# Kernel tuning notes

Hardware: AMD Instinct MI355X
Metric: run time of the kernel (lower is better)

The kernel has to match this reference:

```python
import jax, jax.numpy as jnp
import numpy as np

B, S, D = 2, 4096, 512
H, DK, DV = 8, 64, 64
LN_EPS = 1e-5
ATTN_EPS = 1e-6


def layer_norm(x, g, b):
    mu = jnp.mean(x, axis=-1, keepdims=True)
    var = jnp.var(x, axis=-1, keepdims=True)
    return (x - mu) * jax.lax.rsqrt(var + LN_EPS) * g + b


def setup_inputs() -> dict:
    key = jax.random.key(0)
    ks = jax.random.split(key, 12)
    s = 1.0 / np.sqrt(D)
    inp = {
        "Q": jax.random.normal(ks[0], (B, S, D), jnp.float32),
        "K": jax.random.normal(ks[1], (B, S, D), jnp.float32),
        "V": jax.random.normal(ks[2], (B, S, D), jnp.float32),
        "W_q": jax.random.normal(ks[3], (D, H * DK), jnp.float32) * s,
        "W_k": jax.random.normal(ks[4], (D, H * DK), jnp.float32) * s,
        "W_v": jax.random.normal(ks[5], (D, H * DV), jnp.float32) * s,
        "W_o": jax.random.normal(ks[6], (H * DV, D), jnp.float32) * s,
        "ln1_g": jnp.ones((D,), jnp.float32),
        "ln1_b": jnp.zeros((D,), jnp.float32),
        "ln2_g": jnp.ones((D,), jnp.float32),
        "ln2_b": jnp.zeros((D,), jnp.float32),
        "w1": jax.random.normal(ks[7], (4 * D, D), jnp.float32) * s,  # torch Linear: (out, in)
        "b1": jnp.zeros((4 * D,), jnp.float32),
        "w2": jax.random.normal(ks[8], (D, 4 * D), jnp.float32) * (1.0 / np.sqrt(4 * D)),
        "b2": jnp.zeros((D,), jnp.float32),
    }
    return inp


def reference(Q, K, V, W_q, W_k, W_v, W_o, ln1_g, ln1_b, ln2_g, ln2_b, w1, b1, w2, b2):
    Qn = layer_norm(Q, ln1_g, ln1_b)
    # project and split heads: [B,S,H,dk] -> [B,H,S,dk]
    q = (Qn @ W_q).reshape(B, S, H, DK).transpose(0, 2, 1, 3)
    k = (K @ W_k).reshape(B, S, H, DK).transpose(0, 2, 1, 3)
    v = (V @ W_v).reshape(B, S, H, DV).transpose(0, 2, 1, 3)
    scores = jnp.einsum("bhqd,bhkd->bhqk", q, k) / (np.sqrt(DK) + ATTN_EPS)
    attn = jax.nn.softmax(scores, axis=-1)  # same as max-subtract softmax
    ctx = jnp.einsum("bhqk,bhkd->bhqd", attn, v)
    ctx = ctx.transpose(0, 2, 1, 3).reshape(B, S, H * DV)
    att_out = ctx @ W_o  # dropout = identity (eval)
    X = Q + att_out
    Xn = layer_norm(X, ln2_g, ln2_b)
    h = jax.nn.gelu(Xn @ w1.T + b1, approximate=False)
    ffn = h @ w2.T + b2
    return X + ffn
```

## Files before the change

kernel.cpp:

```cpp
#include <hip/hip_runtime.h>

typedef unsigned short u16;
typedef __attribute__((ext_vector_type(8))) short short8;
typedef __attribute__((ext_vector_type(4))) float f32x4;
typedef __attribute__((ext_vector_type(16))) float f32x16;
typedef __attribute__((ext_vector_type(4))) unsigned u32x4;

struct __align__(8) us4 { u16 x, y, z, w; };
struct __align__(8) ui2 { unsigned x, y; };

#define CEXP (1.44269504089f / (8.0f + 1e-6f))

__device__ __forceinline__ u16 f2bf(float f) {
  unsigned u = __builtin_bit_cast(unsigned, f);
  unsigned r = (u + 0x7FFFu + ((u >> 16) & 1u)) >> 16;
  return (u16)r;
}

__device__ __forceinline__ unsigned pack_bf2_trunc(float a, float b) {
  return __builtin_amdgcn_perm(__builtin_bit_cast(unsigned, b),
                               __builtin_bit_cast(unsigned, a), 0x07060302u);
}

__device__ __forceinline__ void async_load16(const void* g, void* l) {
  __builtin_amdgcn_global_load_lds((const __attribute__((address_space(1))) void*)g,
                                   (__attribute__((address_space(3))) void*)l, 16, 0, 0);
}

__global__ void prep_weights(const float* __restrict__ Wq, const float* __restrict__ Wk,
                             const float* __restrict__ Wv, const float* __restrict__ Wo,
                             const float* __restrict__ w1, const float* __restrict__ w2,
                             u16* __restrict__ wqkvT, u16* __restrict__ woT,
                             u16* __restrict__ w1b, u16* __restrict__ w2b) {
  const int z = blockIdx.y;
  const int stride = gridDim.x * blockDim.x;
  const int i0 = blockIdx.x * blockDim.x + threadIdx.x;
  if (z < 4) {
    const float* src = z == 0 ? Wq : z == 1 ? Wk : z == 2 ? Wv : Wo;
    u16* dst = z < 3 ? wqkvT + z * 512 * 512 : woT;
    const float scale = (z == 0) ? CEXP : 1.0f;
    for (int i = i0; i < 512 * 512; i += stride) {
      int n = i >> 9, k = i & 511;
      dst[i] = f2bf(src[k * 512 + n] * scale);
    }
  } else {
    const float* src = z == 4 ? w1 : w2;
    u16* dst = z == 4 ? w1b : w2b;
    for (int i = i0; i < 2048 * 512; i += stride) dst[i] = f2bf(src[i]);
  }
}

template <bool KV>
__launch_bounds__(128)
__global__ void ln_cast(const float* __restrict__ X, const float* __restrict__ gw,
                        const float* __restrict__ bw, u16* __restrict__ Y,
                        const float* __restrict__ Kin, const float* __restrict__ Vin,
                        u16* __restrict__ Kb, u16* __restrict__ Vb) {
  const int row = blockIdx.x, t = threadIdx.x;
  const size_t base = (size_t)row * 512;
  float4 x = ((const float4*)(X + base))[t];
  float s = x.x + x.y + x.z + x.w;
  float ss = x.x * x.x + x.y * x.y + x.z * x.z + x.w * x.w;
#pragma unroll
  for (int off = 32; off > 0; off >>= 1) {
    s += __shfl_xor(s, off);
    ss += __shfl_xor(ss, off);
  }
  __shared__ float red[4];
  if ((t & 63) == 0) { red[(t >> 6) * 2] = s; red[(t >> 6) * 2 + 1] = ss; }
  __syncthreads();
  const float tot = red[0] + red[2], tss = red[1] + red[3];
  const float mu = tot * (1.0f / 512.0f);
  const float var = tss * (1.0f / 512.0f) - mu * mu;
  const float rs = rsqrtf(var + 1e-5f);
  float4 g4 = ((const float4*)gw)[t];
  float4 b4 = ((const float4*)bw)[t];
  us4 o;
  o.x = f2bf((x.x - mu) * rs * g4.x + b4.x);
  o.y = f2bf((x.y - mu) * rs * g4.y + b4.y);
  o.z = f2bf((x.z - mu) * rs * g4.z + b4.z);
  o.w = f2bf((x.w - mu) * rs * g4.w + b4.w);
  ((us4*)(Y + base))[t] = o;
  if constexpr (KV) {
    float4 k4 = ((const float4*)(Kin + base))[t];
    float4 v4 = ((const float4*)(Vin + base))[t];
    us4 ko, vo;
    ko.x = f2bf(k4.x); ko.y = f2bf(k4.y); ko.z = f2bf(k4.z); ko.w = f2bf(k4.w);
    vo.x = f2bf(v4.x); vo.y = f2bf(v4.y); vo.z = f2bf(v4.z); vo.w = f2bf(v4.w);
    ((us4*)(Kb + base))[t] = ko;
    ((us4*)(Vb + base))[t] = vo;
  }
}

__launch_bounds__(256, 3)
__global__ void gemm_qkv(const u16* __restrict__ Aq, const u16* __restrict__ Ak,
                         const u16* __restrict__ Av, const u16* __restrict__ Bt,
                         u16* __restrict__ qb, u16* __restrict__ kb, u16* __restrict__ vtb) {
  __shared__ __align__(16) u16 sA[128 * 32];
  __shared__ __align__(16) u16 sB[128 * 32];
  const int tid = threadIdx.x;
  const int wave = tid >> 6, lane = tid & 63;
  const int l15 = lane & 15, quad = lane >> 4;
  const int qsw = (quad ^ ((l15 >> 1) & 3)) * 8;
  const int m0 = blockIdx.x * 128, n0 = blockIdx.y * 128;
  const int sel = n0 >> 9;
  const u16* A = sel == 0 ? Aq : sel == 1 ? Ak : Av;
  const int wm = (wave >> 1) * 64, wn = (wave & 1) * 64;
  const int u0 = wave * 64 + lane, u1 = u0 + 256;
  const int sw0 = ((u0 & 3) ^ ((u0 >> 3) & 3)) * 8;
  const int K = 512;

  const u16* a0 = A + (size_t)(m0 + (u0 >> 2)) * K + sw0;
  const u16* a1 = A + (size_t)(m0 + (u1 >> 2)) * K + sw0;
  const u16* b0 = Bt + (size_t)(n0 + (u0 >> 2)) * K + sw0;
  const u16* b1p = Bt + (size_t)(n0 + (u1 >> 2)) * K + sw0;

  f32x4 acc[4][4] = {};
  for (int k0 = 0; k0 < K; k0 += 32) {
    async_load16(a0 + k0, &sA[wave * 512]);
    async_load16(a1 + k0, &sA[2048 + wave * 512]);
    async_load16(b0 + k0, &sB[wave * 512]);
    async_load16(b1p + k0, &sB[2048 + wave * 512]);
    __syncthreads();
    short8 af[4], bfr[4];
#pragma unroll
    for (int i = 0; i < 4; i++)
      af[i] = *(const short8*)&sA[(wm + i * 16 + l15) * 32 + qsw];
#pragma unroll
    for (int j = 0; j < 4; j++)
      bfr[j] = *(const short8*)&sB[(wn + j * 16 + l15) * 32 + qsw];
#pragma unroll
    for (int i = 0; i < 4; i++)
#pragma unroll
      for (int j = 0; j < 4; j++)
        acc[i][j] = __builtin_amdgcn_mfma_f32_16x16x32_bf16(af[i], bfr[j], acc[i][j], 0, 0, 0);
    __syncthreads();
  }

#pragma unroll
  for (int i = 0; i < 4; i++) {
#pragma unroll
    for (int j = 0; j < 4; j++) {
      const int ocol = ((n0 + wn) & 511) + j * 16 + l15;
      const int row0 = m0 + wm + i * 16 + quad * 4;
      if (sel < 2) {
        u16* C = sel == 0 ? qb : kb;
#pragma unroll
        for (int r = 0; r < 4; r++) C[(size_t)(row0 + r) * 512 + ocol] = f2bf(acc[i][j][r]);
      } else {
        const int b = row0 >> 12, s0 = row0 & 4095;
        const int hh = ocol >> 6, cc = ocol & 63;
        us4 pk;
        pk.x = f2bf(acc[i][j][0]); pk.y = f2bf(acc[i][j][1]);
        pk.z = f2bf(acc[i][j][2]); pk.w = f2bf(acc[i][j][3]);
        *(us4*)&vtb[((size_t)((b * 8 + hh) * 64 + cc) << 12) + s0] = pk;
      }
    }
  }
}

template <int EP, int TN, int LB>
__launch_bounds__(256, LB)
__global__ void gemm_bt(const u16* __restrict__ A, const u16* __restrict__ Bt,
                        int M, int N, int K, void* __restrict__ Cp,
                        const float* __restrict__ bias, const float* __restrict__ res) {
  constexpr int MI = (TN == 128) ? 4 : 2;
  __shared__ __align__(16) u16 sA[128 * 32];
  __shared__ __align__(16) u16 sB[TN * 32];
  const int tid = threadIdx.x;
  const int wave = tid >> 6, lane = tid & 63;
  const int l15 = lane & 15, quad = lane >> 4;
  const int qsw = (quad ^ ((l15 >> 1) & 3)) * 8;
  const int m0 = blockIdx.x * 128, n0 = blockIdx.y * TN;
  const int wm = (TN == 128) ? (wave >> 1) * 64 : wave * 32;
  const int wn = (TN == 128) ? (wave & 1) * 64 : 0;
  const int u0 = wave * 64 + lane, u1 = u0 + 256;
  const int sw0 = ((u0 & 3) ^ ((u0 >> 3) & 3)) * 8;

  const u16* a0 = A + (size_t)(m0 + (u0 >> 2)) * K + sw0;
  const u16* a1 = A + (size_t)(m0 + (u1 >> 2)) * K + sw0;
  const u16* b0 = Bt + (size_t)(n0 + (u0 >> 2)) * K + sw0;

  f32x4 acc[MI][4] = {};
  for (int k0 = 0; k0 < K; k0 += 32) {
    async_load16(a0 + k0, &sA[wave * 512]);
    async_load16(a1 + k0, &sA[2048 + wave * 512]);
    async_load16(b0 + k0, &sB[wave * 512]);
    if constexpr (TN == 128) {
      const u16* b1p = Bt + (size_t)(n0 + (u1 >> 2)) * K + sw0;
      async_load16(b1p + k0, &sB[2048 + wave * 512]);
    }
    __syncthreads();
    short8 af[MI], bfr[4];
#pragma unroll
    for (int i = 0; i < MI; i++)
      af[i] = *(const short8*)&sA[(wm + i * 16 + l15) * 32 + qsw];
#pragma unroll
    for (int j = 0; j < 4; j++)
      bfr[j] = *(const short8*)&sB[(wn + j * 16 + l15) * 32 + qsw];
#pragma unroll
    for (int i = 0; i < MI; i++)
#pragma unroll
      for (int j = 0; j < 4; j++)
        acc[i][j] = __builtin_amdgcn_mfma_f32_16x16x32_bf16(af[i], bfr[j], acc[i][j], 0, 0, 0);
    __syncthreads();
  }

#pragma unroll
  for (int i = 0; i < MI; i++) {
#pragma unroll
    for (int j = 0; j < 4; j++) {
      const int col = n0 + wn + j * 16 + l15;
      const int row0 = m0 + wm + i * 16 + quad * 4;
      if (EP == 2) {
        float* C = (float*)Cp;
#pragma unroll
        for (int r = 0; r < 4; r++) {
          size_t idx = (size_t)(row0 + r) * N + col;
          C[idx] = acc[i][j][r] + res[idx];
        }
      } else if (EP == 3) {
        u16* C = (u16*)Cp;
        const float bv = bias[col];
#pragma unroll
        for (int r = 0; r < 4; r++) {
          float xx = acc[i][j][r] + bv;
          float gl = 0.5f * xx * (1.0f + erff(xx * 0.70710678118f));
          C[(size_t)(row0 + r) * N + col] = f2bf(gl);
        }
      } else {
        float* C = (float*)Cp;
        const float bv = bias[col];
#pragma unroll
        for (int r = 0; r < 4; r++) {
          size_t idx = (size_t)(row0 + r) * N + col;
          C[idx] = acc[i][j][r] + bv + res[idx];
        }
      }
    }
  }
}

__launch_bounds__(512, 4)
__global__ void attn_kernel(const u16* __restrict__ qb, const u16* __restrict__ kb,
                            const u16* __restrict__ vtb, u16* __restrict__ ctx) {
  __shared__ __align__(16) u16 sK[2][128 * 64];
  __shared__ __align__(16) u16 sV[2][64 * 128];
  const int tid = threadIdx.x;
  const int wave = tid >> 6, lane = tid & 63;
  const int l31 = lane & 31, hi = lane >> 5;
  const int qg = wave & 3, kh = wave >> 2;
  const int bh = blockIdx.y, b = bh >> 3, h = bh & 7;
  const int q0 = blockIdx.x * 128;
  const size_t rb = (size_t)b * 4096;
  const int qrow = q0 + qg * 32 + l31;

  short8 qf[4];
#pragma unroll
  for (int ks = 0; ks < 4; ks++)
    qf[ks] = *(const short8*)&qb[(rb + qrow) * 512 + h * 64 + ks * 16 + hi * 8];

#define STAGE(bufidx, jj)                                                            \
  {                                                                                  \
    _Pragma("unroll") for (int r = 0; r < 2; r++) {                                  \
      int u = r * 512 + wave * 64 + lane;                                            \
      int row = u >> 3, sl = (u & 7) ^ (row & 7);                                    \
      async_load16(&kb[(rb + (jj) + row) * 512 + h * 64 + sl * 8],                   \
                   &sK[bufidx][(r * 512 + wave * 64) * 8]);                          \
    }                                                                                \
    _Pragma("unroll") for (int r = 0; r < 2; r++) {                                  \
      int u = r * 512 + wave * 64 + lane;                                            \
      int row = u >> 4, sl = (u & 15) ^ (row & 7);                                   \
      async_load16(&vtb[((size_t)(bh * 64 + row)) * 4096 + (jj) + sl * 8],           \
                   &sV[bufidx][(r * 512 + wave * 64) * 8]);                          \
    }                                                                                \
  }

  f32x16 ov[2] = {};
  float l_part = 0.f;

  STAGE(0, 0);
  asm volatile("s_waitcnt vmcnt(0)" ::: "memory");
  __syncthreads();

  for (int t = 0; t < 32; t++) {
    const int cur = t & 1;
    if (t < 31) STAGE(cur ^ 1, (t + 1) * 128);
    const u16* K_ = sK[cur];
    const u16* V_ = sV[cur];
#pragma unroll
    for (int kk2 = 0; kk2 < 2; kk2++) {
      const int kb32 = kh * 2 + kk2;
      f32x16 st = {};
      __builtin_amdgcn_s_setprio(1);
#pragma unroll
      for (int ks = 0; ks < 4; ks++) {
        const int row = kb32 * 32 + l31;
        const int sl = (ks * 2 + hi) ^ (row & 7);
        short8 kf = *(const short8*)&K_[row * 64 + sl * 8];
        st = __builtin_amdgcn_mfma_f32_32x32x16_bf16(kf, qf[ks], st, 0, 0, 0);
      }
      __builtin_amdgcn_s_setprio(0);
      float p[16];
#pragma unroll
      for (int i = 0; i < 16; i++) p[i] = __builtin_amdgcn_exp2f(st[i]);
#pragma unroll
      for (int i = 0; i < 16; i += 4)
        l_part += (p[i] + p[i + 1]) + (p[i + 2] + p[i + 3]);
      unsigned x0 = pack_bf2_trunc(p[0], p[1]), x1 = pack_bf2_trunc(p[2], p[3]);
      unsigned x2 = pack_bf2_trunc(p[4], p[5]), x3 = pack_bf2_trunc(p[6], p[7]);
      unsigned x4 = pack_bf2_trunc(p[8], p[9]), x5 = pack_bf2_trunc(p[10], p[11]);
      unsigned x6 = pack_bf2_trunc(p[12], p[13]), x7 = pack_bf2_trunc(p[14], p[15]);
      auto r0 = __builtin_amdgcn_permlane32_swap(x0, x2, false, false);
      auto r1 = __builtin_amdgcn_permlane32_swap(x1, x3, false, false);
      auto r2 = __builtin_amdgcn_permlane32_swap(x4, x6, false, false);
      auto r3 = __builtin_amdgcn_permlane32_swap(x5, x7, false, false);
      u32x4 w0 = {r0[0], r1[0], r0[1], r1[1]};
      u32x4 w1 = {r2[0], r3[0], r2[1], r3[1]};
      short8 pf0 = __builtin_bit_cast(short8, w0);
      short8 pf1 = __builtin_bit_cast(short8, w1);
      __builtin_amdgcn_s_setprio(1);
#pragma unroll
      for (int vb = 0; vb < 2; vb++) {
        const int row = vb * 32 + l31;
        const int sl0 = (kb32 * 4 + hi) ^ (row & 7);
        const int sl1 = (kb32 * 4 + 2 + hi) ^ (row & 7);
        short8 vf0 = *(const short8*)&V_[row * 128 + sl0 * 8];
        short8 vf1 = *(const short8*)&V_[row * 128 + sl1 * 8];
        ov[vb] = __builtin_amdgcn_mfma_f32_32x32x16_bf16(vf0, pf0, ov[vb], 0, 0, 0);
        ov[vb] = __builtin_amdgcn_mfma_f32_32x32x16_bf16(vf1, pf1, ov[vb], 0, 0, 0);
      }
      __builtin_amdgcn_s_setprio(0);
    }
    asm volatile("s_waitcnt vmcnt(0)" ::: "memory");
    __syncthreads();
  }
#undef STAGE

  float l2 = l_part + __shfl_xor(l_part, 32);
  float* mrg = (float*)&sK[0][0];
  float* mrgl = (float*)&sV[0][0];
  if (kh == 1) {
#pragma unroll
    for (int vb = 0; vb < 2; vb++)
#pragma unroll
      for (int e = 0; e < 16; e++)
        mrg[(qg * 32 + vb * 16 + e) * 64 + lane] = ov[vb][e];
    mrgl[qg * 64 + lane] = l2;
  }
  __syncthreads();
  if (kh == 0) {
    const float inv = 1.0f / (l2 + mrgl[qg * 64 + lane]);
#pragma unroll
    for (int vb = 0; vb < 2; vb++) {
#pragma unroll
      for (int rg = 0; rg < 4; rg++) {
        us4 o;
        o.x = f2bf((ov[vb][rg * 4 + 0] + mrg[(qg * 32 + vb * 16 + rg * 4 + 0) * 64 + lane]) * inv);
        o.y = f2bf((ov[vb][rg * 4 + 1] + mrg[(qg * 32 + vb * 16 + rg * 4 + 1) * 64 + lane]) * inv);
        o.z = f2bf((ov[vb][rg * 4 + 2] + mrg[(qg * 32 + vb * 16 + rg * 4 + 2) * 64 + lane]) * inv);
        o.w = f2bf((ov[vb][rg * 4 + 3] + mrg[(qg * 32 + vb * 16 + rg * 4 + 3) * 64 + lane]) * inv);
        *(us4*)&ctx[(rb + qrow) * 512 + h * 64 + vb * 32 + rg * 8 + hi * 4] = o;
      }
    }
  }
}

extern "C" void kernel_launch(void* const* d_in, const int* in_sizes, int n_in,
                              void* d_out, int out_size, void* d_ws, size_t ws_size,
                              hipStream_t stream) {
  (void)in_sizes; (void)n_in; (void)out_size; (void)ws_size;
  const float* Q = (const float*)d_in[0];
  const float* K = (const float*)d_in[1];
  const float* V = (const float*)d_in[2];
  const float* W_q = (const float*)d_in[3];
  const float* W_k = (const float*)d_in[4];
  const float* W_v = (const float*)d_in[5];
  const float* W_o = (const float*)d_in[6];
  const float* ln1_g = (const float*)d_in[7];
  const float* ln1_b = (const float*)d_in[8];
  const float* ln2_g = (const float*)d_in[9];
  const float* ln2_b = (const float*)d_in[10];
  const float* w1 = (const float*)d_in[11];
  const float* b1 = (const float*)d_in[12];
  const float* w2 = (const float*)d_in[13];
  const float* b2 = (const float*)d_in[14];

  char* w = (char*)d_ws;
  const size_t MB = 1u << 20;
  u16* wqkvT = (u16*)(w);
  u16* woT = (u16*)(w + 3 * MB / 2);
  u16* w1b = (u16*)(w + 2 * MB);
  u16* w2b = (u16*)(w + 4 * MB);
  u16* Qn  = (u16*)(w + 6 * MB);
  u16* Kb  = (u16*)(w + 14 * MB);
  u16* Vb  = (u16*)(w + 22 * MB);
  u16* qb  = (u16*)(w + 30 * MB);
  u16* kb  = (u16*)(w + 38 * MB);
  u16* vtb = (u16*)(w + 46 * MB);
  u16* ctx = (u16*)(w + 54 * MB);
  float* X = (float*)(w + 62 * MB);
  u16* Xn  = (u16*)(w + 6 * MB);
  u16* hb  = (u16*)(w + 14 * MB);

  prep_weights<<<dim3(128, 6), 256, 0, stream>>>(W_q, W_k, W_v, W_o, w1, w2,
                                                 wqkvT, woT, w1b, w2b);
  ln_cast<true><<<8192, 128, 0, stream>>>(Q, ln1_g, ln1_b, Qn, K, V, Kb, Vb);
  gemm_qkv<<<dim3(64, 12), 256, 0, stream>>>(Qn, Kb, Vb, wqkvT, qb, kb, vtb);
  attn_kernel<<<dim3(32, 16), 512, 0, stream>>>(qb, kb, vtb, ctx);
  gemm_bt<2, 64, 3><<<dim3(64, 8), 256, 0, stream>>>(ctx, woT, 8192, 512, 512, X, nullptr, Q);
  ln_cast<false><<<8192, 128, 0, stream>>>(X, ln2_g, ln2_b, Xn, nullptr, nullptr, nullptr, nullptr);
  gemm_bt<3, 128, 3><<<dim3(64, 16), 256, 0, stream>>>(Xn, w1b, 8192, 2048, 512, hb, b1, nullptr);
  gemm_bt<4, 64, 3><<<dim3(64, 8), 256, 0, stream>>>(hb, w2b, 8192, 512, 2048, (float*)d_out, b2, X);
}
```

Baseline: 335.1 us.

## Double query rows per attention block and triple-buffer K/V staging

Each wave in the attention kernel now processes two 32-row query tiles (256 queries per block), so every K/V fragment read from shared memory feeds twice as many MFMAs. The grid is halved and launch bounds are relaxed to allow more registers. K/V staging moves to a three-deep ring with precomputed pointers and partial vmcnt waits, giving loads an extra iteration of lead time. The cost is higher register and LDS use and fewer blocks, which lowers occupancy and may leave CUs idle with only 256 blocks.

```diff
diff --git a/kernel.cpp b/kernel.cpp
--- a/kernel.cpp
+++ b/kernel.cpp
@@ -241,126 +241,169 @@
   }
 }
 
-__launch_bounds__(512, 4)
+__launch_bounds__(512, 2)
 __global__ void attn_kernel(const u16* __restrict__ qb, const u16* __restrict__ kb,
                             const u16* __restrict__ vtb, u16* __restrict__ ctx) {
-  __shared__ __align__(16) u16 sK[2][128 * 64];
-  __shared__ __align__(16) u16 sV[2][64 * 128];
+  __shared__ __align__(16) u16 smem[49152];
   const int tid = threadIdx.x;
   const int wave = tid >> 6, lane = tid & 63;
   const int l31 = lane & 31, hi = lane >> 5;
   const int qg = wave & 3, kh = wave >> 2;
   const int bh = blockIdx.y, b = bh >> 3, h = bh & 7;
-  const int q0 = blockIdx.x * 128;
+  const int q0 = blockIdx.x * 256;
   const size_t rb = (size_t)b * 4096;
-  const int qrow = q0 + qg * 32 + l31;
-
-  short8 qf[4];
-#pragma unroll
-  for (int ks = 0; ks < 4; ks++)
-    qf[ks] = *(const short8*)&qb[(rb + qrow) * 512 + h * 64 + ks * 16 + hi * 8];
-
-#define STAGE(bufidx, jj)                                                            \
-  {                                                                                  \
-    _Pragma("unroll") for (int r = 0; r < 2; r++) {                                  \
-      int u = r * 512 + wave * 64 + lane;                                            \
-      int row = u >> 3, sl = (u & 7) ^ (row & 7);                                    \
-      async_load16(&kb[(rb + (jj) + row) * 512 + h * 64 + sl * 8],                   \
-                   &sK[bufidx][(r * 512 + wave * 64) * 8]);                          \
-    }                                                                                \
-    _Pragma("unroll") for (int r = 0; r < 2; r++) {                                  \
-      int u = r * 512 + wave * 64 + lane;                                            \
-      int row = u >> 4, sl = (u & 15) ^ (row & 7);                                   \
-      async_load16(&vtb[((size_t)(bh * 64 + row)) * 4096 + (jj) + sl * 8],           \
-                   &sV[bufidx][(r * 512 + wave * 64) * 8]);                          \
-    }                                                                                \
-  }
-
-  f32x16 ov[2] = {};
-  float l_part = 0.f;
-
-  STAGE(0, 0);
-  asm volatile("s_waitcnt vmcnt(0)" ::: "memory");
+  const int qrowA = q0 + qg * 64 + l31;
+  const int qrowB = qrowA + 32;
+
+  short8 qfA[4], qfB[4];
+#pragma unroll
+  for (int ks = 0; ks < 4; ks++) {
+    qfA[ks] = *(const short8*)&qb[(rb + qrowA) * 512 + h * 64 + ks * 16 + hi * 8];
+    qfB[ks] = *(const short8*)&qb[(rb + qrowB) * 512 + h * 64 + ks * 16 + hi * 8];
+  }
+
+  const int uk0 = wave * 64 + lane, uk1 = uk0 + 512;
+  const int krow0 = uk0 >> 3, ksl0 = (uk0 & 7) ^ (krow0 & 7);
+  const int krow1 = uk1 >> 3, ksl1 = (uk1 & 7) ^ (krow1 & 7);
+  const u16* kp0 = kb + (rb + krow0) * 512 + h * 64 + ksl0 * 8;
+  const u16* kp1 = kb + (rb + krow1) * 512 + h * 64 + ksl1 * 8;
+  const int vrow0 = uk0 >> 4, vsl0 = (uk0 & 15) ^ (vrow0 & 7);
+  const int vrow1 = uk1 >> 4, vsl1 = (uk1 & 15) ^ (vrow1 & 7);
+  const u16* vp0 = vtb + (size_t)(bh * 64 + vrow0) * 4096 + vsl0 * 8;
+  const u16* vp1 = vtb + (size_t)(bh * 64 + vrow1) * 4096 + vsl1 * 8;
+
+#define STAGE(bi)                                                   \
+  {                                                                 \
+    u16* dK = smem + (bi) * 8192;                                   \
+    u16* dV = smem + 24576 + (bi) * 8192;                           \
+    async_load16(kp0, &dK[(wave * 64) * 8]);                        \
+    async_load16(kp1, &dK[(512 + wave * 64) * 8]);                  \
+    async_load16(vp0, &dV[(wave * 64) * 8]);                        \
+    async_load16(vp1, &dV[(512 + wave * 64) * 8]);                  \
+    kp0 += 128 * 512; kp1 += 128 * 512; vp0 += 128; vp1 += 128;     \
+  }
+
+  f32x16 ovA[2] = {}, ovB[2] = {};
+  float lA = 0.f, lB = 0.f;
+
+  STAGE(0);
+  STAGE(1);
+  asm volatile("s_waitcnt vmcnt(4)" ::: "memory");
   __syncthreads();
 
   for (int t = 0; t < 32; t++) {
-    const int cur = t & 1;
-    if (t < 31) STAGE(cur ^ 1, (t + 1) * 128);
-    const u16* K_ = sK[cur];
-    const u16* V_ = sV[cur];
+    const int cur = t % 3;
+    if (t < 30) STAGE((t + 2) % 3);
+    const u16* K_ = smem + cur * 8192;
+    const u16* V_ = smem + 24576 + cur * 8192;
 #pragma unroll
     for (int kk2 = 0; kk2 < 2; kk2++) {
       const int kb32 = kh * 2 + kk2;
-      f32x16 st = {};
+      f32x16 stA = {}, stB = {};
       __builtin_amdgcn_s_setprio(1);
 #pragma unroll
       for (int ks = 0; ks < 4; ks++) {
         const int row = kb32 * 32 + l31;
-        const int sl = (ks * 2 + hi) ^ (row & 7);
+        const int sl = (ks * 2 + hi) ^ (l31 & 7);
         short8 kf = *(const short8*)&K_[row * 64 + sl * 8];
-        st = __builtin_amdgcn_mfma_f32_32x32x16_bf16(kf, qf[ks], st, 0, 0, 0);
+        stA = __builtin_amdgcn_mfma_f32_32x32x16_bf16(kf, qfA[ks], stA, 0, 0, 0);
+        stB = __builtin_amdgcn_mfma_f32_32x32x16_bf16(kf, qfB[ks], stB, 0, 0, 0);
       }
       __builtin_amdgcn_s_setprio(0);
-      float p[16];
-#pragma unroll
-      for (int i = 0; i < 16; i++) p[i] = __builtin_amdgcn_exp2f(st[i]);
-#pragma unroll
-      for (int i = 0; i < 16; i += 4)
-        l_part += (p[i] + p[i + 1]) + (p[i + 2] + p[i + 3]);
-      unsigned x0 = pack_bf2_trunc(p[0], p[1]), x1 = pack_bf2_trunc(p[2], p[3]);
-      unsigned x2 = pack_bf2_trunc(p[4], p[5]), x3 = pack_bf2_trunc(p[6], p[7]);
-      unsigned x4 = pack_bf2_trunc(p[8], p[9]), x5 = pack_bf2_trunc(p[10], p[11]);
-      unsigned x6 = pack_bf2_trunc(p[12], p[13]), x7 = pack_bf2_trunc(p[14], p[15]);
-      auto r0 = __builtin_amdgcn_permlane32_swap(x0, x2, false, false);
-      auto r1 = __builtin_amdgcn_permlane32_swap(x1, x3, false, false);
-      auto r2 = __builtin_amdgcn_permlane32_swap(x4, x6, false, false);
-      auto r3 = __builtin_amdgcn_permlane32_swap(x5, x7, false, false);
-      u32x4 w0 = {r0[0], r1[0], r0[1], r1[1]};
-      u32x4 w1 = {r2[0], r3[0], r2[1], r3[1]};
-      short8 pf0 = __builtin_bit_cast(short8, w0);
-      short8 pf1 = __builtin_bit_cast(short8, w1);
+      float pA[16], pB[16];
+#pragma unroll
+      for (int i = 0; i < 16; i++) pA[i] = __builtin_amdgcn_exp2f(stA[i]);
+#pragma unroll
+      for (int i = 0; i < 16; i++) pB[i] = __builtin_amdgcn_exp2f(stB[i]);
+#pragma unroll
+      for (int i = 0; i < 16; i += 4) {
+        lA += (pA[i] + pA[i + 1]) + (pA[i + 2] + pA[i + 3]);
+        lB += (pB[i] + pB[i + 1]) + (pB[i + 2] + pB[i + 3]);
+      }
+      unsigned a0 = pack_bf2_trunc(pA[0], pA[1]), a1 = pack_bf2_trunc(pA[2], pA[3]);
+      unsigned a2 = pack_bf2_trunc(pA[4], pA[5]), a3 = pack_bf2_trunc(pA[6], pA[7]);
+      unsigned a4 = pack_bf2_trunc(pA[8], pA[9]), a5 = pack_bf2_trunc(pA[10], pA[11]);
+      unsigned a6 = pack_bf2_trunc(pA[12], pA[13]), a7 = pack_bf2_trunc(pA[14], pA[15]);
+      auto ra0 = __builtin_amdgcn_permlane32_swap(a0, a2, false, false);
+      auto ra1 = __builtin_amdgcn_permlane32_swap(a1, a3, false, false);
+      auto ra2 = __builtin_amdgcn_permlane32_swap(a4, a6, false, false);
+      auto ra3 = __builtin_amdgcn_permlane32_swap(a5, a7, false, false);
+      u32x4 wa0 = {ra0[0], ra1[0], ra0[1], ra1[1]};
+      u32x4 wa1 = {ra2[0], ra3[0], ra2[1], ra3[1]};
+      short8 pfA0 = __builtin_bit_cast(short8, wa0);
+      short8 pfA1 = __builtin_bit_cast(short8, wa1);
+      unsigned b0 = pack_bf2_trunc(pB[0], pB[1]), b1 = pack_bf2_trunc(pB[2], pB[3]);
+      unsigned b2 = pack_bf2_trunc(pB[4], pB[5]), b3 = pack_bf2_trunc(pB[6], pB[7]);
+      unsigned b4 = pack_bf2_trunc(pB[8], pB[9]), b5 = pack_bf2_trunc(pB[10], pB[11]);
+      unsigned b6 = pack_bf2_trunc(pB[12], pB[13]), b7 = pack_bf2_trunc(pB[14], pB[15]);
+      auto rb0 = __builtin_amdgcn_permlane32_swap(b0, b2, false, false);
+      auto rb1 = __builtin_amdgcn_permlane32_swap(b1, b3, false, false);
+      auto rb2 = __builtin_amdgcn_permlane32_swap(b4, b6, false, false);
+      auto rb3 = __builtin_amdgcn_permlane32_swap(b5, b7, false, false);
+      u32x4 wb0 = {rb0[0], rb1[0], rb0[1], rb1[1]};
+      u32x4 wb1 = {rb2[0], rb3[0], rb2[1], rb3[1]};
+      short8 pfB0 = __builtin_bit_cast(short8, wb0);
+      short8 pfB1 = __builtin_bit_cast(short8, wb1);
       __builtin_amdgcn_s_setprio(1);
 #pragma unroll
       for (int vb = 0; vb < 2; vb++) {
         const int row = vb * 32 + l31;
-        const int sl0 = (kb32 * 4 + hi) ^ (row & 7);
-        const int sl1 = (kb32 * 4 + 2 + hi) ^ (row & 7);
+        const int sl0 = (kb32 * 4 + hi) ^ (l31 & 7);
+        const int sl1 = (kb32 * 4 + 2 + hi) ^ (l31 & 7);
         short8 vf0 = *(const short8*)&V_[row * 128 + sl0 * 8];
         short8 vf1 = *(const short8*)&V_[row * 128 + sl1 * 8];
-        ov[vb] = __builtin_amdgcn_mfma_f32_32x32x16_bf16(vf0, pf0, ov[vb], 0, 0, 0);
-        ov[vb] = __builtin_amdgcn_mfma_f32_32x32x16_bf16(vf1, pf1, ov[vb], 0, 0, 0);
+        ovA[vb] = __builtin_amdgcn_mfma_f32_32x32x16_bf16(vf0, pfA0, ovA[vb], 0, 0, 0);
+        ovA[vb] = __builtin_amdgcn_mfma_f32_32x32x16_bf16(vf1, pfA1, ovA[vb], 0, 0, 0);
+        ovB[vb] = __builtin_amdgcn_mfma_f32_32x32x16_bf16(vf0, pfB0, ovB[vb], 0, 0, 0);
+        ovB[vb] = __builtin_amdgcn_mfma_f32_32x32x16_bf16(vf1, pfB1, ovB[vb], 0, 0, 0);
       }
       __builtin_amdgcn_s_setprio(0);
     }
-    asm volatile("s_waitcnt vmcnt(0)" ::: "memory");
-    __syncthreads();
+    if (t < 31) {
+      if (t < 30)
+        asm volatile("s_waitcnt vmcnt(4)" ::: "memory");
+      else
+        asm volatile("s_waitcnt vmcnt(0)" ::: "memory");
+      __syncthreads();
+    }
   }
 #undef STAGE
 
-  float l2 = l_part + __shfl_xor(l_part, 32);
-  float* mrg = (float*)&sK[0][0];
-  float* mrgl = (float*)&sV[0][0];
+  float l2A = lA + __shfl_xor(lA, 32);
+  float l2B = lB + __shfl_xor(lB, 32);
+  __syncthreads();
+  float* mrg = (float*)&smem[0];
+  float* mrgl = (float*)&smem[32768];
   if (kh == 1) {
 #pragma unroll
     for (int vb = 0; vb < 2; vb++)
 #pragma unroll
-      for (int e = 0; e < 16; e++)
-        mrg[(qg * 32 + vb * 16 + e) * 64 + lane] = ov[vb][e];
-    mrgl[qg * 64 + lane] = l2;
+      for (int e = 0; e < 16; e++) {
+        mrg[((qg * 2 + 0) * 32 + vb * 16 + e) * 64 + lane] = ovA[vb][e];
+        mrg[((qg * 2 + 1) * 32 + vb * 16 + e) * 64 + lane] = ovB[vb][e];
+      }
+    mrgl[(qg * 2 + 0) * 64 + lane] = l2A;
+    mrgl[(qg * 2 + 1) * 64 + lane] = l2B;
   }
   __syncthreads();
   if (kh == 0) {
-    const float inv = 1.0f / (l2 + mrgl[qg * 64 + lane]);
+    const float invA = 1.0f / (l2A + mrgl[(qg * 2 + 0) * 64 + lane]);
+    const float invB = 1.0f / (l2B + mrgl[(qg * 2 + 1) * 64 + lane]);
 #pragma unroll
     for (int vb = 0; vb < 2; vb++) {
 #pragma unroll
       for (int rg = 0; rg < 4; rg++) {
-        us4 o;
-        o.x = f2bf((ov[vb][rg * 4 + 0] + mrg[(qg * 32 + vb * 16 + rg * 4 + 0) * 64 + lane]) * inv);
-        o.y = f2bf((ov[vb][rg * 4 + 1] + mrg[(qg * 32 + vb * 16 + rg * 4 + 1) * 64 + lane]) * inv);
-        o.z = f2bf((ov[vb][rg * 4 + 2] + mrg[(qg * 32 + vb * 16 + rg * 4 + 2) * 64 + lane]) * inv);
-        o.w = f2bf((ov[vb][rg * 4 + 3] + mrg[(qg * 32 + vb * 16 + rg * 4 + 3) * 64 + lane]) * inv);
-        *(us4*)&ctx[(rb + qrow) * 512 + h * 64 + vb * 32 + rg * 8 + hi * 4] = o;
+        us4 oA, oB;
+        oA.x = f2bf((ovA[vb][rg * 4 + 0] + mrg[((qg * 2 + 0) * 32 + vb * 16 + rg * 4 + 0) * 64 + lane]) * invA);
+        oA.y = f2bf((ovA[vb][rg * 4 + 1] + mrg[((qg * 2 + 0) * 32 + vb * 16 + rg * 4 + 1) * 64 + lane]) * invA);
+        oA.z = f2bf((ovA[vb][rg * 4 + 2] + mrg[((qg * 2 + 0) * 32 + vb * 16 + rg * 4 + 2) * 64 + lane]) * invA);
+        oA.w = f2bf((ovA[vb][rg * 4 + 3] + mrg[((qg * 2 + 0) * 32 + vb * 16 + rg * 4 + 3) * 64 + lane]) * invA);
+        *(us4*)&ctx[(rb + qrowA) * 512 + h * 64 + vb * 32 + rg * 8 + hi * 4] = oA;
+        oB.x = f2bf((ovB[vb][rg * 4 + 0] + mrg[((qg * 2 + 1) * 32 + vb * 16 + rg * 4 + 0) * 64 + lane]) * invB);
+        oB.y = f2bf((ovB[vb][rg * 4 + 1] + mrg[((qg * 2 + 1) * 32 + vb * 16 + rg * 4 + 1) * 64 + lane]) * invB);
+        oB.z = f2bf((ovB[vb][rg * 4 + 2] + mrg[((qg * 2 + 1) * 32 + vb * 16 + rg * 4 + 2) * 64 + lane]) * invB);
+        oB.w = f2bf((ovB[vb][rg * 4 + 3] + mrg[((qg * 2 + 1) * 32 + vb * 16 + rg * 4 + 3) * 64 + lane]) * invB);
+        *(us4*)&ctx[(rb + qrowB) * 512 + h * 64 + vb * 32 + rg * 8 + hi * 4] = oB;
       }
     }
   }
@@ -407,7 +450,7 @@
                                                  wqkvT, woT, w1b, w2b);
   ln_cast<true><<<8192, 128, 0, stream>>>(Q, ln1_g, ln1_b, Qn, K, V, Kb, Vb);
   gemm_qkv<<<dim3(64, 12), 256, 0, stream>>>(Qn, Kb, Vb, wqkvT, qb, kb, vtb);
-  attn_kernel<<<dim3(32, 16), 512, 0, stream>>>(qb, kb, vtb, ctx);
+  attn_kernel<<<dim3(16, 16), 512, 0, stream>>>(qb, kb, vtb, ctx);
   gemm_bt<2, 64, 3><<<dim3(64, 8), 256, 0, stream>>>(ctx, woT, 8192, 512, 512, X, nullptr, Q);
   ln_cast<false><<<8192, 128, 0, stream>>>(X, ln2_g, ln2_b, Xn, nullptr, nullptr, nullptr, nullptr);
   gemm_bt<3, 128, 3><<<dim3(64, 16), 256, 0, stream>>>(Xn, w1b, 8192, 2048, 512, hb, b1, nullptr);
```

Result: faster. 322.8 us (-3.7%).

## Triple-buffer attention K/V tiles in 64-key chunks with wait-one prefetch

Applied to the files above, without the earlier changes.

Restructures the attention kernel's K/V staging from double-buffered 128-key tiles to triple-buffered 64-key tiles. The loop now waits only on the oldest outstanding load (vmcnt(2)) so two prefetches stay in flight. The wave mapping changes so each wave handles 32 keys per tile, and the grid axes are swapped so consecutive blocks share a head. It also lowers the launch-bounds occupancy hint from 4 to 2, which relaxes the register limit but adds one barrier per 64 keys, twice as many as before.

```diff
diff --git a/kernel.cpp b/kernel.cpp
--- a/kernel.cpp
+++ b/kernel.cpp
@@ -241,17 +241,16 @@
   }
 }
 
-__launch_bounds__(512, 4)
+__launch_bounds__(512, 2)
 __global__ void attn_kernel(const u16* __restrict__ qb, const u16* __restrict__ kb,
                             const u16* __restrict__ vtb, u16* __restrict__ ctx) {
-  __shared__ __align__(16) u16 sK[2][128 * 64];
-  __shared__ __align__(16) u16 sV[2][64 * 128];
+  __shared__ __align__(16) u16 smem[24576];
   const int tid = threadIdx.x;
   const int wave = tid >> 6, lane = tid & 63;
   const int l31 = lane & 31, hi = lane >> 5;
-  const int qg = wave & 3, kh = wave >> 2;
-  const int bh = blockIdx.y, b = bh >> 3, h = bh & 7;
-  const int q0 = blockIdx.x * 128;
+  const int qg = wave >> 1, kh = wave & 1;
+  const int bh = blockIdx.x, b = bh >> 3, h = bh & 7;
+  const int q0 = blockIdx.y * 128;
   const size_t rb = (size_t)b * 4096;
   const int qrow = q0 + qg * 32 + l31;
 
@@ -260,86 +259,88 @@
   for (int ks = 0; ks < 4; ks++)
     qf[ks] = *(const short8*)&qb[(rb + qrow) * 512 + h * 64 + ks * 16 + hi * 8];
 
-#define STAGE(bufidx, jj)                                                            \
-  {                                                                                  \
-    _Pragma("unroll") for (int r = 0; r < 2; r++) {                                  \
-      int u = r * 512 + wave * 64 + lane;                                            \
-      int row = u >> 3, sl = (u & 7) ^ (row & 7);                                    \
-      async_load16(&kb[(rb + (jj) + row) * 512 + h * 64 + sl * 8],                   \
-                   &sK[bufidx][(r * 512 + wave * 64) * 8]);                          \
-    }                                                                                \
-    _Pragma("unroll") for (int r = 0; r < 2; r++) {                                  \
-      int u = r * 512 + wave * 64 + lane;                                            \
-      int row = u >> 4, sl = (u & 15) ^ (row & 7);                                   \
-      async_load16(&vtb[((size_t)(bh * 64 + row)) * 4096 + (jj) + sl * 8],           \
-                   &sV[bufidx][(r * 512 + wave * 64) * 8]);                          \
-    }                                                                                \
+  const int srow = tid >> 3, ssl = (tid & 7) ^ (srow & 7);
+  const u16* kp = kb + (rb + srow) * 512 + h * 64 + ssl * 8;
+  const u16* vp = vtb + (size_t)(bh * 64 + srow) * 4096 + ssl * 8;
+
+#define STAGE(bi)                                  \
+  {                                                \
+    async_load16(kp, &smem[(bi) * 4096 + tid * 8]);\
+    async_load16(vp, &smem[12288 + (bi) * 4096 + tid * 8]); \
+    kp += 64 * 512; vp += 64;                      \
   }
 
   f32x16 ov[2] = {};
   float l_part = 0.f;
 
-  STAGE(0, 0);
-  asm volatile("s_waitcnt vmcnt(0)" ::: "memory");
+  STAGE(0);
+  STAGE(1);
+  asm volatile("s_waitcnt vmcnt(2)" ::: "memory");
   __syncthreads();
 
-  for (int t = 0; t < 32; t++) {
-    const int cur = t & 1;
-    if (t < 31) STAGE(cur ^ 1, (t + 1) * 128);
-    const u16* K_ = sK[cur];
-    const u16* V_ = sV[cur];
-#pragma unroll
-    for (int kk2 = 0; kk2 < 2; kk2++) {
-      const int kb32 = kh * 2 + kk2;
-      f32x16 st = {};
-      __builtin_amdgcn_s_setprio(1);
-#pragma unroll
-      for (int ks = 0; ks < 4; ks++) {
-        const int row = kb32 * 32 + l31;
-        const int sl = (ks * 2 + hi) ^ (row & 7);
-        short8 kf = *(const short8*)&K_[row * 64 + sl * 8];
-        st = __builtin_amdgcn_mfma_f32_32x32x16_bf16(kf, qf[ks], st, 0, 0, 0);
-      }
-      __builtin_amdgcn_s_setprio(0);
-      float p[16];
-#pragma unroll
-      for (int i = 0; i < 16; i++) p[i] = __builtin_amdgcn_exp2f(st[i]);
-#pragma unroll
-      for (int i = 0; i < 16; i += 4)
-        l_part += (p[i] + p[i + 1]) + (p[i + 2] + p[i + 3]);
-      unsigned x0 = pack_bf2_trunc(p[0], p[1]), x1 = pack_bf2_trunc(p[2], p[3]);
-      unsigned x2 = pack_bf2_trunc(p[4], p[5]), x3 = pack_bf2_trunc(p[6], p[7]);
-      unsigned x4 = pack_bf2_trunc(p[8], p[9]), x5 = pack_bf2_trunc(p[10], p[11]);
-      unsigned x6 = pack_bf2_trunc(p[12], p[13]), x7 = pack_bf2_trunc(p[14], p[15]);
-      auto r0 = __builtin_amdgcn_permlane32_swap(x0, x2, false, false);
-      auto r1 = __builtin_amdgcn_permlane32_swap(x1, x3, false, false);
-      auto r2 = __builtin_amdgcn_permlane32_swap(x4, x6, false, false);
-      auto r3 = __builtin_amdgcn_permlane32_swap(x5, x7, false, false);
-      u32x4 w0 = {r0[0], r1[0], r0[1], r1[1]};
-      u32x4 w1 = {r2[0], r3[0], r2[1], r3[1]};
-      short8 pf0 = __builtin_bit_cast(short8, w0);
-      short8 pf1 = __builtin_bit_cast(short8, w1);
-      __builtin_amdgcn_s_setprio(1);
-#pragma unroll
-      for (int vb = 0; vb < 2; vb++) {
-        const int row = vb * 32 + l31;
-        const int sl0 = (kb32 * 4 + hi) ^ (row & 7);
-        const int sl1 = (kb32 * 4 + 2 + hi) ^ (row & 7);
-        short8 vf0 = *(const short8*)&V_[row * 128 + sl0 * 8];
-        short8 vf1 = *(const short8*)&V_[row * 128 + sl1 * 8];
-        ov[vb] = __builtin_amdgcn_mfma_f32_32x32x16_bf16(vf0, pf0, ov[vb], 0, 0, 0);
-        ov[vb] = __builtin_amdgcn_mfma_f32_32x32x16_bf16(vf1, pf1, ov[vb], 0, 0, 0);
-      }
-      __builtin_amdgcn_s_setprio(0);
-    }
-    asm volatile("s_waitcnt vmcnt(0)" ::: "memory");
-    __syncthreads();
+  int cur = 0, nxt = 2;
+  for (int t = 0; t < 64; t++) {
+    if (t < 62) {
+      STAGE(nxt);
+      nxt = nxt == 2 ? 0 : nxt + 1;
+    }
+    const u16* K_ = smem + cur * 4096;
+    const u16* V_ = smem + 12288 + cur * 4096;
+    cur = cur == 2 ? 0 : cur + 1;
+    f32x16 st = {};
+    __builtin_amdgcn_s_setprio(1);
+#pragma unroll
+    for (int ks = 0; ks < 4; ks++) {
+      const int row = kh * 32 + l31;
+      const int sl = (ks * 2 + hi) ^ (row & 7);
+      short8 kf = *(const short8*)&K_[row * 64 + sl * 8];
+      st = __builtin_amdgcn_mfma_f32_32x32x16_bf16(kf, qf[ks], st, 0, 0, 0);
+    }
+    __builtin_amdgcn_s_setprio(0);
+    float p[16];
+#pragma unroll
+    for (int i = 0; i < 16; i++) p[i] = __builtin_amdgcn_exp2f(st[i]);
+#pragma unroll
+    for (int i = 0; i < 16; i += 4)
+      l_part += (p[i] + p[i + 1]) + (p[i + 2] + p[i + 3]);
+    unsigned x0 = pack_bf2_trunc(p[0], p[1]), x1 = pack_bf2_trunc(p[2], p[3]);
+    unsigned x2 = pack_bf2_trunc(p[4], p[5]), x3 = pack_bf2_trunc(p[6], p[7]);
+    unsigned x4 = pack_bf2_trunc(p[8], p[9]), x5 = pack_bf2_trunc(p[10], p[11]);
+    unsigned x6 = pack_bf2_trunc(p[12], p[13]), x7 = pack_bf2_trunc(p[14], p[15]);
+    auto r0 = __builtin_amdgcn_permlane32_swap(x0, x2, false, false);
+    auto r1 = __builtin_amdgcn_permlane32_swap(x1, x3, false, false);
+    auto r2 = __builtin_amdgcn_permlane32_swap(x4, x6, false, false);
+    auto r3 = __builtin_amdgcn_permlane32_swap(x5, x7, false, false);
+    u32x4 w0 = {r0[0], r1[0], r0[1], r1[1]};
+    u32x4 w1 = {r2[0], r3[0], r2[1], r3[1]};
+    short8 pf0 = __builtin_bit_cast(short8, w0);
+    short8 pf1 = __builtin_bit_cast(short8, w1);
+    __builtin_amdgcn_s_setprio(1);
+#pragma unroll
+    for (int vb = 0; vb < 2; vb++) {
+      const int row = vb * 32 + l31;
+      const int sl0 = (kh * 4 + hi) ^ (row & 7);
+      const int sl1 = (kh * 4 + 2 + hi) ^ (row & 7);
+      short8 vf0 = *(const short8*)&V_[row * 64 + sl0 * 8];
+      short8 vf1 = *(const short8*)&V_[row * 64 + sl1 * 8];
+      ov[vb] = __builtin_amdgcn_mfma_f32_32x32x16_bf16(vf0, pf0, ov[vb], 0, 0, 0);
+      ov[vb] = __builtin_amdgcn_mfma_f32_32x32x16_bf16(vf1, pf1, ov[vb], 0, 0, 0);
+    }
+    __builtin_amdgcn_s_setprio(0);
+    if (t < 63) {
+      if (t < 62)
+        asm volatile("s_waitcnt vmcnt(2)" ::: "memory");
+      else
+        asm volatile("s_waitcnt vmcnt(0)" ::: "memory");
+      __syncthreads();
+    }
   }
 #undef STAGE
 
   float l2 = l_part + __shfl_xor(l_part, 32);
-  float* mrg = (float*)&sK[0][0];
-  float* mrgl = (float*)&sV[0][0];
+  __syncthreads();
+  float* mrg = (float*)smem;
+  float* mrgl = (float*)smem + 8192;
   if (kh == 1) {
 #pragma unroll
     for (int vb = 0; vb < 2; vb++)
@@ -407,7 +408,7 @@
                                                  wqkvT, woT, w1b, w2b);
   ln_cast<true><<<8192, 128, 0, stream>>>(Q, ln1_g, ln1_b, Qn, K, V, Kb, Vb);
   gemm_qkv<<<dim3(64, 12), 256, 0, stream>>>(Qn, Kb, Vb, wqkvT, qb, kb, vtb);
-  attn_kernel<<<dim3(32, 16), 512, 0, stream>>>(qb, kb, vtb, ctx);
+  attn_kernel<<<dim3(16, 32), 512, 0, stream>>>(qb, kb, vtb, ctx);
   gemm_bt<2, 64, 3><<<dim3(64, 8), 256, 0, stream>>>(ctx, woT, 8192, 512, 512, X, nullptr, Q);
   ln_cast<false><<<8192, 128, 0, stream>>>(X, ln2_g, ln2_b, Xn, nullptr, nullptr, nullptr, nullptr);
   gemm_bt<3, 128, 3><<<dim3(64, 16), 256, 0, stream>>>(Xn, w1b, 8192, 2048, 512, hb, b1, nullptr);
```

Measured after the change: 328.6 us. Within noise of the previous version (-1.9%).
